# Kernel optimization log

Hardware: AMD Instinct MI355X
Metric: run time of the kernel (lower is better)

The kernel has to match this reference:

```python
import jax, jax.numpy as jnp
import numpy as np

N_NODES = 70000
N_EDGES = 2_000_000
IN_CH, FEAT_CH, OUT_CH = 1044, 128, 3


def _gcn_norm(src_sl, dst_sl, n_nodes, dtype):
    # PyG gcn_norm with add_self_loops=True, edge_weight=1:
    # deg over target nodes, norm = deg^-1/2[src] * deg^-1/2[dst]
    deg = jax.ops.segment_sum(jnp.ones(src_sl.shape[0], dtype=dtype), dst_sl,
                              num_segments=n_nodes)
    dinv = jnp.where(deg > 0, jax.lax.rsqrt(deg), jnp.zeros((), dtype))
    return dinv[src_sl] * dinv[dst_sl]


def _gcn_layer(x, src_sl, dst_sl, norm, W, b, n_nodes):
    h = x @ W                                  # [N, out] linear transform first
    msg = h[src_sl] * norm[:, None]            # gather + scale
    out = jax.ops.segment_sum(msg, dst_sl, num_segments=n_nodes)  # scatter-add
    return out + b


def setup_inputs() -> dict:
    key = jax.random.key(0)
    ks = jax.random.split(key, 6)
    features = jax.random.normal(ks[0], (N_NODES, IN_CH), dtype=jnp.float32)
    edges = jax.random.randint(ks[1], (2, N_EDGES), 0, N_NODES, dtype=jnp.int64)
    edges2 = jax.random.randint(ks[2], (2, N_EDGES), 0, N_NODES, dtype=jnp.int64)
    edge_features = jax.random.normal(ks[3], (N_EDGES,), dtype=jnp.float32)
    W1 = jax.random.normal(ks[4], (IN_CH, FEAT_CH), dtype=jnp.float32) * (1.0 / np.sqrt(IN_CH))
    b1 = jnp.zeros((FEAT_CH,), dtype=jnp.float32)
    W2 = jax.random.normal(ks[5], (FEAT_CH, OUT_CH), dtype=jnp.float32) * (1.0 / np.sqrt(FEAT_CH))
    b2 = jnp.zeros((OUT_CH,), dtype=jnp.float32)
    return {"features": features, "edges": edges, "edges2": edges2,
            "edge_features": edge_features, "W1": W1, "b1": b1, "W2": W2, "b2": b2}


def reference(features, edges, edges2, edge_features, W1, b1, W2, b2):
    # edge_features is discarded by the module (set to None); edges2 unused.
    n = features.shape[0]
    loop = jnp.arange(n, dtype=edges.dtype)
    src_sl = jnp.concatenate([edges[0], loop])  # self-loops appended
    dst_sl = jnp.concatenate([edges[1], loop])
    norm = _gcn_norm(src_sl, dst_sl, n, features.dtype)
    x = _gcn_layer(features, src_sl, dst_sl, norm, W1, b1, n)
    x = jax.nn.relu(x)
    # dropout is identity in eval mode (deterministic reference)
    return _gcn_layer(x, src_sl, dst_sl, norm, W2, b2, n)
```

## Files before the change

kernel.cpp:

```cpp
#include <hip/hip_runtime.h>
#include <hip/hip_bf16.h>

#define K_IN   1044
#define N_FEAT 128
#define KPAD2  1088
#define NST2   17
#define BM     96

#define NB     512
#define BWMAX  256
#define EPB    8192

typedef __attribute__((ext_vector_type(8))) short short8;
typedef __attribute__((ext_vector_type(4))) float f32x4;

__device__ __forceinline__ ushort f2bf(float f) {
  unsigned x = __float_as_uint(f);
  x += 0x7fffu + ((x >> 16) & 1u);
  return (ushort)(x >> 16);
}
__device__ __forceinline__ uint pkbf(float lo, float hi) {
  __hip_bfloat162 h = __float22bfloat162_rn(make_float2(lo, hi));
  return *reinterpret_cast<uint*>(&h);
}
__device__ __forceinline__ float bflo(uint v) { return __uint_as_float(v << 16); }
__device__ __forceinline__ float bfhi(uint v) { return __uint_as_float(v & 0xFFFF0000u); }

__device__ __forceinline__ void gld16(const void* g, void* l) {
  __builtin_amdgcn_global_load_lds(
      (const __attribute__((address_space(1))) unsigned int*)g,
      (__attribute__((address_space(3))) unsigned int*)l, 16, 0, 0);
}


__global__ __launch_bounds__(256) void convw1_hist_kernel(const float* __restrict__ W1,
                                                          ushort* __restrict__ W1T,
                                                          const int* __restrict__ dst,
                                                          int* __restrict__ pbc,
                                                          int E, int bw, int convBlocks,
                                                          int eblocks) {
  if ((int)blockIdx.x < convBlocks) {
    int idx = blockIdx.x * 256 + threadIdx.x;
    if (idx >= N_FEAT * KPAD2) return;
    int col = idx / KPAD2, k = idx - col * KPAD2;
    int kk = k & ~63;
    int jp = (k >> 3) & 7;
    int e  = k & 7;
    int jl = jp ^ (col & 7);
    int ksrc = kk + 8 * jl + e;
    W1T[idx] = (ksrc < K_IN) ? f2bf(W1[(size_t)ksrc * N_FEAT + col]) : (ushort)0;
  } else {
    __shared__ int h[NB];
    const int t = threadIdx.x;
    const int blk = blockIdx.x - convBlocks;
    for (int i = t; i < NB; i += 256) h[i] = 0;
    __syncthreads();
    const int e0 = blk * EPB;
    const int e1 = min(e0 + EPB, E);
    for (int e = e0 + t; e < e1; e += 256) atomicAdd(&h[dst[e] / bw], 1);
    __syncthreads();
    for (int i = t; i < NB; i += 256) pbc[i * eblocks + blk] = h[i];
  }
}

__global__ __launch_bounds__(256) void csr_scan_bucket_kernel(int* __restrict__ pbc,
                                                              int* __restrict__ bt,
                                                              int eblocks) {
  __shared__ int sc[256];
  const int b = blockIdx.x;
  const int t = threadIdx.x;
  int v = (t < eblocks) ? pbc[(size_t)b * eblocks + t] : 0;
  sc[t] = v;
  __syncthreads();
  for (int off = 1; off < 256; off <<= 1) {
    int x = (t >= off) ? sc[t - off] : 0;
    __syncthreads();
    sc[t] += x;
    __syncthreads();
  }
  if (t < eblocks) pbc[(size_t)b * eblocks + t] = sc[t] - v;
  if (t == 255) bt[b] = sc[255];
}

__global__ __launch_bounds__(256) void csr_bucket_scan_kernel(const int* __restrict__ bt,
                                                              int* __restrict__ bucket_base) {
  __shared__ int sc[256];
  const int t = threadIdx.x;
  int v0 = bt[2 * t], v1 = bt[2 * t + 1];
  int s = v0 + v1;
  sc[t] = s;
  __syncthreads();
  for (int off = 1; off < 256; off <<= 1) {
    int x = (t >= off) ? sc[t - off] : 0;
    __syncthreads();
    sc[t] += x;
    __syncthreads();
  }
  int excl = sc[t] - s;
  bucket_base[2 * t]     = excl;
  bucket_base[2 * t + 1] = excl + v0;
  if (t == 255) bucket_base[NB] = sc[255];
}

__global__ __launch_bounds__(256) void csr_stage_kernel(const int* __restrict__ src,
                                                        const int* __restrict__ dst,
                                                        const int* __restrict__ pbc,
                                                        const int* __restrict__ bucket_base,
                                                        uint* __restrict__ staging, int E, int bw,
                                                        int eblocks) {
  __shared__ int cur[NB];
  const int t = threadIdx.x;
  const int blk = blockIdx.x;
  for (int i = t; i < NB; i += 256)
    cur[i] = bucket_base[i] + pbc[(size_t)i * eblocks + blk];
  __syncthreads();
  const int e0 = blk * EPB;
  const int e1 = min(e0 + EPB, E);
  for (int e = e0 + t; e < e1; e += 256) {
    int d = dst[e];
    int b = d / bw;
    int p = atomicAdd(&cur[b], 1);
    staging[p] = ((uint)src[e] << 8) | (uint)(d - b * bw);
  }
}

__global__ __launch_bounds__(256) void csr_final_kernel(const uint* __restrict__ staging,
                                                        const int* __restrict__ bucket_base,
                                                        int* __restrict__ row_ptr,
                                                        int* __restrict__ sorted_src,
                                                        float* __restrict__ dinv,
                                                        int N, int bw, int E) {
  __shared__ int hist[BWMAX];
  __shared__ int sc[256];
  const int b = blockIdx.x;
  const int t = threadIdx.x;
  if (b == 0 && t == 0) row_ptr[N] = E;
  const int node0 = b * bw;
  const int nn = min(bw, N - node0);
  if (nn <= 0) return;
  const int base = bucket_base[b];
  const int cnt  = bucket_base[b + 1] - base;

  for (int i = t; i < BWMAX; i += 256) hist[i] = 0;
  __syncthreads();
  for (int i = t; i < cnt; i += 256)
    atomicAdd(&hist[staging[base + i] & 255u], 1);
  __syncthreads();
  int v = (t < nn) ? hist[t] : 0;
  if (t < nn) dinv[node0 + t] = rsqrtf((float)(v + 1));
  sc[t] = v;
  __syncthreads();
  for (int off = 1; off < 256; off <<= 1) {
    int x = (t >= off) ? sc[t - off] : 0;
    __syncthreads();
    sc[t] += x;
    __syncthreads();
  }
  int excl = sc[t] - v;
  if (t < nn) row_ptr[node0 + t] = base + excl;
  if (t < nn) hist[t] = excl;
  __syncthreads();
  for (int i = t; i < cnt; i += 256) {
    uint p = staging[base + i];
    int c = atomicAdd(&hist[p & 255u], 1);
    sorted_src[base + c] = (int)(p >> 8);
  }
}


__global__ __launch_bounds__(256) void gemm1_mfma_kernel(const float* __restrict__ X,
                                                         const ushort* __restrict__ W1T,
                                                         const float* __restrict__ dinv,
                                                         ushort* __restrict__ G1, int M) {
  __shared__ float  Af[2][BM * 64];
  __shared__ ushort Bsb[2][128 * 64];

  const int t = threadIdx.x;
  const int row0 = blockIdx.x * BM;
  const int w = t >> 6, l = t & 63;
  const int w24 = w * 24, w32 = w * 32;
  const int Mm1 = M - 1;

  const int wm = w >> 1, wn = w & 1;
  const int lr = l & 15, g = l >> 4;

  f32x4 acc[3][4] = {};

  auto stage = [&](int s, int buf) {
    const int kk = s * 64;
    #pragma unroll
    for (int i = 0; i < 6; i++) {
      int r  = w24 + 4 * i + (l >> 4);
      int jl = (l & 15) ^ (r & 15);
      int grow = min(row0 + r, Mm1);
      int gk   = min(kk + 4 * jl, K_IN - 4);
      gld16(X + (size_t)grow * K_IN + gk, (void*)&Af[buf][(w24 + 4 * i) * 64]);
    }
    #pragma unroll
    for (int i = 0; i < 4; i++) {
      int c = w32 + 8 * i + (l >> 3);
      gld16(W1T + (size_t)c * KPAD2 + kk + 8 * (l & 7),
            (void*)&Bsb[buf][(w32 + 8 * i) * 64]);
    }
  };

  stage(0, 0);
  __syncthreads();

  int cur = 0;
  #pragma unroll 1
  for (int s = 0; s < NST2; s++) {
    if (s + 1 < NST2) stage(s + 1, cur ^ 1);

    #pragma unroll
    for (int ss = 0; ss < 2; ss++) {
      short8 af[3], bfr[4];
      #pragma unroll
      for (int m = 0; m < 3; m++) {
        const int row = wm * 48 + m * 16 + lr;
        const float* rp = &Af[cur][row * 64];
        const int c0 = (ss * 8 + 2 * g)     ^ (row & 15);
        const int c1 = (ss * 8 + 2 * g + 1) ^ (row & 15);
        float4 a0 = *(const float4*)&rp[c0 * 4];
        float4 a1 = *(const float4*)&rp[c1 * 4];
        uint4 uu = make_uint4(pkbf(a0.x, a0.y), pkbf(a0.z, a0.w),
                              pkbf(a1.x, a1.y), pkbf(a1.z, a1.w));
        af[m] = *(short8*)&uu;
      }
      #pragma unroll
      for (int n = 0; n < 4; n++) {
        const int col = wn * 64 + n * 16 + lr;
        const int cB = (ss * 4 + g) ^ (col & 7);
        bfr[n] = *(const short8*)&Bsb[cur][col * 64 + cB * 8];
      }
      #pragma unroll
      for (int m = 0; m < 3; m++)
        #pragma unroll
        for (int n = 0; n < 4; n++)
          acc[m][n] = __builtin_amdgcn_mfma_f32_16x16x32_bf16(af[m], bfr[n], acc[m][n], 0, 0, 0);
    }

    __syncthreads();
    cur ^= 1;
  }

  const int rbase = row0 + wm * 48 + g * 4;
  const int cbase = wn * 64 + lr;
  #pragma unroll
  for (int m = 0; m < 3; m++) {
    #pragma unroll
    for (int r = 0; r < 4; r++) {
      int row = rbase + m * 16 + r;
      if (row < M) {
        float dv = dinv[row];
        #pragma unroll
        for (int n = 0; n < 4; n++)
          G1[(size_t)row * N_FEAT + cbase + n * 16] = f2bf(dv * acc[m][n][r]);
      }
    }
  }
}


__global__ __launch_bounds__(256) void agg1mm_kernel(const ushort* __restrict__ G1,
                                                     const int* __restrict__ row_ptr,
                                                     const int* __restrict__ sorted_src,
                                                     const float* __restrict__ dinv,
                                                     const float* __restrict__ b1,
                                                     const float* __restrict__ W2,
                                                     float* __restrict__ G2, int N) {
  const int w = (blockIdx.x * blockDim.x + threadIdx.x) >> 6;
  const int lane = threadIdx.x & 63;
  if (w >= N) return;
  const int beg = row_ptr[w], end = row_ptr[w + 1];
  const uint* g1u = (const uint*)G1;
  const int co = lane;

  uint vs = g1u[((size_t)w << 6) + co];
  float a0 = bflo(vs), a1 = bfhi(vs);

  int e = beg;
  for (; e + 16 <= end; e += 16) {
    int s[16];
    #pragma unroll
    for (int i = 0; i < 16; i++) s[i] = sorted_src[e + i];
    uint v[16];
    #pragma unroll
    for (int i = 0; i < 16; i++) v[i] = g1u[((size_t)s[i] << 6) + co];
    #pragma unroll
    for (int i = 0; i < 16; i++) { a0 += bflo(v[i]); a1 += bfhi(v[i]); }
  }
  for (; e + 4 <= end; e += 4) {
    int s[4];
    #pragma unroll
    for (int i = 0; i < 4; i++) s[i] = sorted_src[e + i];
    uint v[4];
    #pragma unroll
    for (int i = 0; i < 4; i++) v[i] = g1u[((size_t)s[i] << 6) + co];
    #pragma unroll
    for (int i = 0; i < 4; i++) { a0 += bflo(v[i]); a1 += bfhi(v[i]); }
  }
  for (; e < end; e++) {
    uint v = g1u[((size_t)sorted_src[e] << 6) + co];
    a0 += bflo(v); a1 += bfhi(v);
  }

  const float di = dinv[w];
  float r0 = fmaxf(fmaf(di, a0, b1[2 * co + 0]), 0.f);
  float r1 = fmaxf(fmaf(di, a1, b1[2 * co + 1]), 0.f);

  const float* wrow = W2 + 6 * co;
  float s0 = r0 * wrow[0] + r1 * wrow[3];
  float s1 = r0 * wrow[1] + r1 * wrow[4];
  float s2 = r0 * wrow[2] + r1 * wrow[5];
  #pragma unroll
  for (int off = 32; off > 0; off >>= 1) {
    s0 += __shfl_down(s0, off);
    s1 += __shfl_down(s1, off);
    s2 += __shfl_down(s2, off);
  }
  if (lane == 0) {
    *(float4*)&G2[(size_t)w * 4] = make_float4(di * s0, di * s1, di * s2, 0.f);
  }
}


__global__ __launch_bounds__(256) void agg2_kernel(const float* __restrict__ G2,
                                                   const int* __restrict__ row_ptr,
                                                   const int* __restrict__ sorted_src,
                                                   const float* __restrict__ dinv,
                                                   const float* __restrict__ b2,
                                                   float* __restrict__ out, int N) {
  int t = blockIdx.x * blockDim.x + threadIdx.x;
  int node = t >> 5, lane = t & 31;
  if (node >= N) return;
  int beg = row_ptr[node], end = row_ptr[node + 1];
  float a0 = 0.f, a1 = 0.f, a2 = 0.f;
  for (int e = beg + lane; e < end; e += 32) {
    float4 v = *(const float4*)&G2[(size_t)sorted_src[e] * 4];
    a0 += v.x; a1 += v.y; a2 += v.z;
  }
  #pragma unroll
  for (int off = 16; off > 0; off >>= 1) {
    a0 += __shfl_down(a0, off, 32);
    a1 += __shfl_down(a1, off, 32);
    a2 += __shfl_down(a2, off, 32);
  }
  if (lane == 0) {
    float di = dinv[node];
    float4 self = *(const float4*)&G2[(size_t)node * 4];
    out[node * 3 + 0] = di * (a0 + self.x) + b2[0];
    out[node * 3 + 1] = di * (a1 + self.y) + b2[1];
    out[node * 3 + 2] = di * (a2 + self.z) + b2[2];
  }
}


extern "C" void kernel_launch(void* const* d_in, const int* in_sizes, int n_in,
                              void* d_out, int out_size, void* d_ws, size_t ws_size,
                              hipStream_t stream) {
  const float* features = (const float*)d_in[0];
  const int*   edges    = (const int*)d_in[1];
  const float* W1 = (const float*)d_in[4];
  const float* b1 = (const float*)d_in[5];
  const float* W2 = (const float*)d_in[6];
  const float* b2 = (const float*)d_in[7];
  float* out = (float*)d_out;

  const int N = in_sizes[0] / K_IN;
  const int E = in_sizes[1] / 2;
  const int* src = edges;
  const int* dst = edges + E;
  const int bw = (N + NB - 1) / NB;

  char* ws = (char*)d_ws;
  size_t off = 0;
  auto alloc = [&](size_t bytes) {
    void* p = ws + off;
    off += (bytes + 255) & ~(size_t)255;
    return p;
  };
  const int eblocks = (E + EPB - 1) / EPB;

  int*    pbc           = (int*)   alloc((size_t)NB * eblocks * sizeof(int));
  int*    bt            = (int*)   alloc((size_t)NB * sizeof(int));
  int*    bucket_base   = (int*)   alloc((size_t)(NB + 1) * sizeof(int));
  int*    row_ptr       = (int*)   alloc((size_t)(N + 1) * sizeof(int));
  float*  dinv          = (float*) alloc((size_t)N * sizeof(float));
  uint*   staging       = (uint*)  alloc((size_t)E * sizeof(uint));
  int*    sorted_src    = (int*)   alloc((size_t)E * sizeof(int));
  ushort* G1            = (ushort*)alloc((size_t)N * N_FEAT * sizeof(ushort));
  float*  G2            = (float*) alloc((size_t)N * 4 * sizeof(float));
  ushort* W1T           = (ushort*)alloc((size_t)N_FEAT * KPAD2 * sizeof(ushort));
  (void)ws_size;

  const int convBlocks = (N_FEAT * KPAD2 + 255) / 256;

  convw1_hist_kernel<<<convBlocks + eblocks, 256, 0, stream>>>(W1, W1T, dst, pbc, E, bw, convBlocks, eblocks);
  csr_scan_bucket_kernel<<<NB, 256, 0, stream>>>(pbc, bt, eblocks);
  csr_bucket_scan_kernel<<<1, 256, 0, stream>>>(bt, bucket_base);
  csr_stage_kernel<<<eblocks, 256, 0, stream>>>(src, dst, pbc, bucket_base, staging, E, bw, eblocks);
  csr_final_kernel<<<NB, 256, 0, stream>>>(staging, bucket_base, row_ptr, sorted_src, dinv, N, bw, E);
  gemm1_mfma_kernel<<<(N + BM - 1) / BM, 256, 0, stream>>>(features, W1T, dinv, G1, N);
  agg1mm_kernel<<<((size_t)N * 64 + 255) / 256, 256, 0, stream>>>(G1, row_ptr, sorted_src, dinv, b1, W2, G2, N);
  agg2_kernel<<<((size_t)N * 32 + 255) / 256, 256, 0, stream>>>(G2, row_ptr, sorted_src, dinv, b2, out, N);
}
```

Before: 236.2 us.

## Fold bucket scan into stage/final kernels, use magic-multiply division, narrow agg2 groups

Removes the single-block bucket-scan launch. Each stage and final block now recomputes the 512-entry bucket prefix sum redundantly in shared memory, which saves one dependent launch at the cost of a small repeated scan. Integer division by the bucket width is replaced with a precomputed umulhi magic multiply. agg2 now uses 16 lanes per node instead of 32, which cuts idle lanes for the average degree of roughly 29. The magic-multiply division is exact only when the node count stays within the range its precomputed constant covers.

```diff
diff --git a/kernel.cpp b/kernel.cpp
--- a/kernel.cpp
+++ b/kernel.cpp
@@ -26,6 +26,8 @@
 __device__ __forceinline__ float bflo(uint v) { return __uint_as_float(v << 16); }
 __device__ __forceinline__ float bfhi(uint v) { return __uint_as_float(v & 0xFFFF0000u); }
 
+__device__ __forceinline__ uint divbw(uint d, uint M32) { return __umulhi(d, M32); }
+
 __device__ __forceinline__ void gld16(const void* g, void* l) {
   __builtin_amdgcn_global_load_lds(
       (const __attribute__((address_space(1))) unsigned int*)g,
@@ -37,8 +39,8 @@
                                                           ushort* __restrict__ W1T,
                                                           const int* __restrict__ dst,
                                                           int* __restrict__ pbc,
-                                                          int E, int bw, int convBlocks,
-                                                          int eblocks) {
+                                                          int E, int bw, uint M32,
+                                                          int convBlocks, int eblocks) {
   if ((int)blockIdx.x < convBlocks) {
     int idx = blockIdx.x * 256 + threadIdx.x;
     if (idx >= N_FEAT * KPAD2) return;
@@ -57,7 +59,7 @@
     __syncthreads();
     const int e0 = blk * EPB;
     const int e1 = min(e0 + EPB, E);
-    for (int e = e0 + t; e < e1; e += 256) atomicAdd(&h[dst[e] / bw], 1);
+    for (int e = e0 + t; e < e1; e += 256) atomicAdd(&h[divbw((uint)dst[e], M32)], 1);
     __syncthreads();
     for (int i = t; i < NB; i += 256) pbc[i * eblocks + blk] = h[i];
   }
@@ -82,10 +84,16 @@
   if (t == 255) bt[b] = sc[255];
 }
 
-__global__ __launch_bounds__(256) void csr_bucket_scan_kernel(const int* __restrict__ bt,
-                                                              int* __restrict__ bucket_base) {
+__global__ __launch_bounds__(256) void csr_stage_kernel(const int* __restrict__ src,
+                                                        const int* __restrict__ dst,
+                                                        const int* __restrict__ pbc,
+                                                        const int* __restrict__ bt,
+                                                        uint* __restrict__ staging, int E, int bw,
+                                                        uint M32, int eblocks) {
   __shared__ int sc[256];
+  __shared__ int cur[NB];
   const int t = threadIdx.x;
+  const int blk = blockIdx.x;
   int v0 = bt[2 * t], v1 = bt[2 * t + 1];
   int s = v0 + v1;
   sc[t] = s;
@@ -97,49 +105,54 @@
     __syncthreads();
   }
   int excl = sc[t] - s;
-  bucket_base[2 * t]     = excl;
-  bucket_base[2 * t + 1] = excl + v0;
-  if (t == 255) bucket_base[NB] = sc[255];
-}
-
-__global__ __launch_bounds__(256) void csr_stage_kernel(const int* __restrict__ src,
-                                                        const int* __restrict__ dst,
-                                                        const int* __restrict__ pbc,
-                                                        const int* __restrict__ bucket_base,
-                                                        uint* __restrict__ staging, int E, int bw,
-                                                        int eblocks) {
-  __shared__ int cur[NB];
-  const int t = threadIdx.x;
-  const int blk = blockIdx.x;
-  for (int i = t; i < NB; i += 256)
-    cur[i] = bucket_base[i] + pbc[(size_t)i * eblocks + blk];
+  cur[2 * t]     = excl      + pbc[(size_t)(2 * t) * eblocks + blk];
+  cur[2 * t + 1] = excl + v0 + pbc[(size_t)(2 * t + 1) * eblocks + blk];
   __syncthreads();
   const int e0 = blk * EPB;
   const int e1 = min(e0 + EPB, E);
   for (int e = e0 + t; e < e1; e += 256) {
     int d = dst[e];
-    int b = d / bw;
+    int b = (int)divbw((uint)d, M32);
     int p = atomicAdd(&cur[b], 1);
     staging[p] = ((uint)src[e] << 8) | (uint)(d - b * bw);
   }
 }
 
 __global__ __launch_bounds__(256) void csr_final_kernel(const uint* __restrict__ staging,
-                                                        const int* __restrict__ bucket_base,
+                                                        const int* __restrict__ bt,
                                                         int* __restrict__ row_ptr,
                                                         int* __restrict__ sorted_src,
                                                         float* __restrict__ dinv,
                                                         int N, int bw, int E) {
   __shared__ int hist[BWMAX];
   __shared__ int sc[256];
+  __shared__ int bb[NB];
   const int b = blockIdx.x;
   const int t = threadIdx.x;
   if (b == 0 && t == 0) row_ptr[N] = E;
+
+  {
+    int v0 = bt[2 * t], v1 = bt[2 * t + 1];
+    int s = v0 + v1;
+    sc[t] = s;
+    __syncthreads();
+    for (int off = 1; off < 256; off <<= 1) {
+      int x = (t >= off) ? sc[t - off] : 0;
+      __syncthreads();
+      sc[t] += x;
+      __syncthreads();
+    }
+    int excl = sc[t] - s;
+    bb[2 * t]     = excl;
+    bb[2 * t + 1] = excl + v0;
+    __syncthreads();
+  }
+
   const int node0 = b * bw;
   const int nn = min(bw, N - node0);
   if (nn <= 0) return;
-  const int base = bucket_base[b];
-  const int cnt  = bucket_base[b + 1] - base;
+  const int base = bb[b];
+  const int cnt  = bt[b];
 
   for (int i = t; i < BWMAX; i += 256) hist[i] = 0;
   __syncthreads();
@@ -332,19 +345,19 @@
                                                    const float* __restrict__ b2,
                                                    float* __restrict__ out, int N) {
   int t = blockIdx.x * blockDim.x + threadIdx.x;
-  int node = t >> 5, lane = t & 31;
+  int node = t >> 4, lane = t & 15;
   if (node >= N) return;
   int beg = row_ptr[node], end = row_ptr[node + 1];
   float a0 = 0.f, a1 = 0.f, a2 = 0.f;
-  for (int e = beg + lane; e < end; e += 32) {
+  for (int e = beg + lane; e < end; e += 16) {
     float4 v = *(const float4*)&G2[(size_t)sorted_src[e] * 4];
     a0 += v.x; a1 += v.y; a2 += v.z;
   }
   #pragma unroll
-  for (int off = 16; off > 0; off >>= 1) {
-    a0 += __shfl_down(a0, off, 32);
-    a1 += __shfl_down(a1, off, 32);
-    a2 += __shfl_down(a2, off, 32);
+  for (int off = 8; off > 0; off >>= 1) {
+    a0 += __shfl_down(a0, off, 16);
+    a1 += __shfl_down(a1, off, 16);
+    a2 += __shfl_down(a2, off, 16);
   }
   if (lane == 0) {
     float di = dinv[node];
@@ -372,6 +385,7 @@
   const int* src = edges;
   const int* dst = edges + E;
   const int bw = (N + NB - 1) / NB;
+  const uint M32 = (uint)((0x100000000ULL + (unsigned long long)bw - 1) / (unsigned long long)bw);
 
   char* ws = (char*)d_ws;
   size_t off = 0;
@@ -384,7 +398,6 @@
 
   int*    pbc           = (int*)   alloc((size_t)NB * eblocks * sizeof(int));
   int*    bt            = (int*)   alloc((size_t)NB * sizeof(int));
-  int*    bucket_base   = (int*)   alloc((size_t)(NB + 1) * sizeof(int));
   int*    row_ptr       = (int*)   alloc((size_t)(N + 1) * sizeof(int));
   float*  dinv          = (float*) alloc((size_t)N * sizeof(float));
   uint*   staging       = (uint*)  alloc((size_t)E * sizeof(uint));
@@ -396,12 +409,11 @@
 
   const int convBlocks = (N_FEAT * KPAD2 + 255) / 256;
 
-  convw1_hist_kernel<<<convBlocks + eblocks, 256, 0, stream>>>(W1, W1T, dst, pbc, E, bw, convBlocks, eblocks);
+  convw1_hist_kernel<<<convBlocks + eblocks, 256, 0, stream>>>(W1, W1T, dst, pbc, E, bw, M32, convBlocks, eblocks);
   csr_scan_bucket_kernel<<<NB, 256, 0, stream>>>(pbc, bt, eblocks);
-  csr_bucket_scan_kernel<<<1, 256, 0, stream>>>(bt, bucket_base);
-  csr_stage_kernel<<<eblocks, 256, 0, stream>>>(src, dst, pbc, bucket_base, staging, E, bw, eblocks);
-  csr_final_kernel<<<NB, 256, 0, stream>>>(staging, bucket_base, row_ptr, sorted_src, dinv, N, bw, E);
+  csr_stage_kernel<<<eblocks, 256, 0, stream>>>(src, dst, pbc, bt, staging, E, bw, M32, eblocks);
+  csr_final_kernel<<<NB, 256, 0, stream>>>(staging, bt, row_ptr, sorted_src, dinv, N, bw, E);
   gemm1_mfma_kernel<<<(N + BM - 1) / BM, 256, 0, stream>>>(features, W1T, dinv, G1, N);
   agg1mm_kernel<<<((size_t)N * 64 + 255) / 256, 256, 0, stream>>>(G1, row_ptr, sorted_src, dinv, b1, W2, G2, N);
-  agg2_kernel<<<((size_t)N * 32 + 255) / 256, 256, 0, stream>>>(G2, row_ptr, sorted_src, dinv, b2, out, N);
-}
+  agg2_kernel<<<((size_t)N * 16 + 255) / 256, 256, 0, stream>>>(G2, row_ptr, sorted_src, dinv, b2, out, N);
+}
```

Measured after the change: 234.0 us (median of 2 runs). About the same (-0.9%).
